# Performance work log

Hardware: AMD Instinct MI355X
Metric: run time of the kernel (lower is better)

Reference implementation:

```python
import jax, jax.numpy as jnp
import numpy as np

N_RBF = 16
N_HIDDEN = 64
CUTOFF = 5.0
N_ATOMS = 4096


def setup_inputs() -> dict:
    key = jax.random.key(0)
    ks = jax.random.split(key, 7)
    # Scale positions so the 5.0 cutoff yields a sparse-ish neighbor graph.
    positions = jax.random.normal(ks[0], (N_ATOMS, 3), dtype=jnp.float32) * 10.0
    s1 = 1.0 / np.sqrt(N_RBF)
    s2 = 1.0 / np.sqrt(N_HIDDEN)
    W1 = jax.random.normal(ks[1], (N_RBF, N_HIDDEN), dtype=jnp.float32) * s1
    b1 = jax.random.normal(ks[2], (N_HIDDEN,), dtype=jnp.float32) * 0.01
    W2 = jax.random.normal(ks[3], (N_HIDDEN, N_HIDDEN), dtype=jnp.float32) * s2
    b2 = jax.random.normal(ks[4], (N_HIDDEN,), dtype=jnp.float32) * 0.01
    W3 = jax.random.normal(ks[5], (N_HIDDEN, 1), dtype=jnp.float32) * s2
    b3 = jax.random.normal(ks[6], (1,), dtype=jnp.float32) * 0.01
    return {"positions": positions, "W1": W1, "b1": b1, "W2": W2, "b2": b2, "W3": W3, "b3": b3}


def _features(positions):
    # positions: (N, 3) -> per-node RBF-aggregated features (N, n_rbf).
    # Equivalent to torch mask.nonzero + scatter_add: features[i] = sum_j in-cutoff rbf(d_ij).
    diff = positions[:, None, :] - positions[None, :, :]          # (N, N, 3)
    dist = jnp.sqrt(jnp.sum(diff * diff, axis=-1))                # (N, N)
    mask = (dist > 1e-6) & (dist < CUTOFF)                        # (N, N)
    centers = jnp.linspace(0.5, CUTOFF, N_RBF, dtype=jnp.float32) # (n_rbf,)
    eta = 0.5 * CUTOFF / N_RBF
    gauss = jnp.exp(-((dist[..., None] - centers) ** 2) / (2.0 * eta * eta))  # (N, N, n_rbf)
    x = jnp.minimum(dist / CUTOFF, 1.0)
    smooth = 0.5 * (1.0 + jnp.cos(jnp.float32(np.pi) * x))        # (N, N)
    w = jnp.where(mask, smooth, 0.0)                              # masked smooth-cutoff weight
    return jnp.einsum('ij,ijk->ik', w, gauss)                     # (N, n_rbf)


def reference(positions, W1, b1, W2, b2, W3, b3):
    feats = _features(positions)                                  # (N, n_rbf)
    h = jax.nn.silu(feats @ W1 + b1)
    h = jax.nn.silu(h @ W2 + b2)
    energy = jnp.sum(h @ W3 + b3)                                 # scalar
    return energy
```

## Files before the change

### kernel.cpp

```cpp
#include <hip/hip_runtime.h>

#define N_ATOMS  4096
#define N_RBF    16
#define N_HIDDEN 64
#define NTHREADS 512
#define WPB      8
#define NBLOCKS  (N_ATOMS / WPB)
#define QCAP     256

__global__ void zero_out_kernel(float* __restrict__ out) {
    if (threadIdx.x == 0 && blockIdx.x == 0) out[0] = 0.0f;
}

__device__ __forceinline__ void accum_rbf(float d2, float (&f)[N_RBF]) {
    const float d  = sqrtf(d2);
    const float sm = 0.5f + 0.5f * __cosf(0.62831853071795865f * d);
    #pragma unroll
    for (int k = 0; k < N_RBF; ++k) {
        const float t = d - (0.5f + 0.3f * (float)k);
        f[k] += sm * __expf(-20.48f * t * t);
    }
}

__device__ __forceinline__ int wave_prefix(unsigned long long m) {
    return __builtin_amdgcn_mbcnt_hi((unsigned)(m >> 32),
            __builtin_amdgcn_mbcnt_lo((unsigned)m, 0u));
}

__global__ __launch_bounds__(NTHREADS, 4) void fused_sr_kernel(
    const float* __restrict__ pos,
    const float* __restrict__ W1,
    const float* __restrict__ b1,
    const float* __restrict__ W2,
    const float* __restrict__ b2,
    const float* __restrict__ W3,
    const float* __restrict__ b3,
    float* __restrict__ out)
{
    __shared__ __align__(16) float4 sp[N_ATOMS];
    __shared__ float qd[WPB][QCAP];
    __shared__ __align__(16) float h1buf[WPB][N_HIDDEN];
    __shared__ float ered[WPB];

    const int tid = threadIdx.x;

    for (int idx = tid; idx < N_ATOMS; idx += NTHREADS) {
        sp[idx] = make_float4(pos[idx * 3 + 0], pos[idx * 3 + 1], pos[idx * 3 + 2], 0.0f);
    }
    __syncthreads();

    const int lane = tid & 63;
    const int wib  = tid >> 6;
    const int i    = blockIdx.x * WPB + wib;

    const float4 pi4 = sp[i];
    const float xi = pi4.x, yi = pi4.y, zi = pi4.z;

    int cnt = 0;
    #pragma unroll 8
    for (int j0 = 0; j0 < N_ATOMS; j0 += 64) {
        const float4 pj = sp[j0 + lane];
        const float dx = xi - pj.x;
        const float dy = yi - pj.y;
        const float dz = zi - pj.z;
        const float d2 = fmaf(dx, dx, fmaf(dy, dy, dz * dz));
        const bool act = (d2 < 25.0f) && (d2 > 1e-12f);
        const unsigned long long m = __ballot(act);
        int widx = cnt + wave_prefix(m);
        widx = widx < QCAP ? widx : QCAP - 1;
        if (act) qd[wib][widx] = d2;
        cnt += (int)__popcll(m);
    }

    float f[N_RBF];
    #pragma unroll
    for (int k = 0; k < N_RBF; ++k) f[k] = 0.0f;
    for (int b = 0; b < cnt; b += 64) {
        const int q = b + lane;
        accum_rbf((q < cnt) ? qd[wib][q] : 1e8f, f);
    }

    #pragma unroll
    for (int k = 0; k < N_RBF; ++k) {
        #pragma unroll
        for (int off = 32; off > 0; off >>= 1)
            f[k] += __shfl_xor(f[k], off, 64);
    }

    float a1 = b1[lane];
    #pragma unroll
    for (int k = 0; k < N_RBF; ++k)
        a1 = fmaf(f[k], W1[k * N_HIDDEN + lane], a1);
    const float h1 = a1 / (1.0f + __expf(-a1));

    h1buf[wib][lane] = h1;
    float a2 = b2[lane];
    #pragma unroll
    for (int k = 0; k < N_HIDDEN; k += 4) {
        const float4 hv = *reinterpret_cast<const float4*>(&h1buf[wib][k]);
        a2 = fmaf(hv.x, W2[(k + 0) * N_HIDDEN + lane], a2);
        a2 = fmaf(hv.y, W2[(k + 1) * N_HIDDEN + lane], a2);
        a2 = fmaf(hv.z, W2[(k + 2) * N_HIDDEN + lane], a2);
        a2 = fmaf(hv.w, W2[(k + 3) * N_HIDDEN + lane], a2);
    }
    const float h2 = a2 / (1.0f + __expf(-a2));

    float energy = h2 * W3[lane];
    #pragma unroll
    for (int off = 32; off > 0; off >>= 1)
        energy += __shfl_xor(energy, off, 64);
    if (lane == 0) ered[wib] = energy;
    __syncthreads();
    if (tid == 0) {
        float e = 0.0f;
        #pragma unroll
        for (int w = 0; w < WPB; ++w) e += ered[w];
        atomicAdd(out, e + (float)WPB * b3[0]);
    }
}

extern "C" void kernel_launch(void* const* d_in, const int* in_sizes, int n_in,
                              void* d_out, int out_size, void* d_ws, size_t ws_size,
                              hipStream_t stream) {
    const float* pos = (const float*)d_in[0];
    const float* W1  = (const float*)d_in[1];
    const float* b1  = (const float*)d_in[2];
    const float* W2  = (const float*)d_in[3];
    const float* b2  = (const float*)d_in[4];
    const float* W3  = (const float*)d_in[5];
    const float* b3  = (const float*)d_in[6];
    float* out = (float*)d_out;

    zero_out_kernel<<<1, 64, 0, stream>>>(out);
    fused_sr_kernel<<<NBLOCKS, NTHREADS, 0, stream>>>(pos, W1, b1, W2, b2, W3, b3, out);
}
```

Before: 84.08 us.

## Split each atom's neighbor scan across two waves per atom

Each atom's neighbor scan over all positions is split between two waves, each covering half of the j range. The block grows to 1024 threads and still handles 8 atoms, so the block count is unchanged. Partial RBF sums meet in shared memory, and only the first wave of each pair runs the MLP. The intent is to halve the serial scan per wave and raise the number of resident waves for latency hiding. In exchange it adds an extra block barrier, shrinks the per-wave queue capacity and tightens the launch bounds, which may pressure registers.

```diff
diff --git a/kernel.cpp b/kernel.cpp
--- a/kernel.cpp
+++ b/kernel.cpp
@@ -3,10 +3,12 @@
 #define N_ATOMS  4096
 #define N_RBF    16
 #define N_HIDDEN 64
-#define NTHREADS 512
-#define WPB      8
-#define NBLOCKS  (N_ATOMS / WPB)
-#define QCAP     256
+#define NTHREADS 1024
+#define WPB      16
+#define APB      8
+#define NBLOCKS  (N_ATOMS / APB)
+#define QCAP     192
+#define HALF_J   (N_ATOMS / 2)
 
 __global__ void zero_out_kernel(float* __restrict__ out) {
     if (threadIdx.x == 0 && blockIdx.x == 0) out[0] = 0.0f;
@@ -27,7 +29,7 @@
             __builtin_amdgcn_mbcnt_lo((unsigned)m, 0u));
 }
 
-__global__ __launch_bounds__(NTHREADS, 4) void fused_sr_kernel(
+__global__ __launch_bounds__(NTHREADS, 8) void fused_sr_kernel(
     const float* __restrict__ pos,
     const float* __restrict__ W1,
     const float* __restrict__ b1,
@@ -38,9 +40,9 @@
     float* __restrict__ out)
 {
     __shared__ __align__(16) float4 sp[N_ATOMS];
-    __shared__ float qd[WPB][QCAP];
-    __shared__ __align__(16) float h1buf[WPB][N_HIDDEN];
-    __shared__ float ered[WPB];
+    __shared__ __align__(16) float qd[WPB][QCAP];
+    __shared__ float pairbuf[APB][2][N_RBF];
+    __shared__ float ered[APB];
 
     const int tid = threadIdx.x;
 
@@ -51,15 +53,18 @@
 
     const int lane = tid & 63;
     const int wib  = tid >> 6;
-    const int i    = blockIdx.x * WPB + wib;
+    const int pid  = wib >> 1;
+    const int half = wib & 1;
+    const int i    = blockIdx.x * APB + pid;
 
     const float4 pi4 = sp[i];
     const float xi = pi4.x, yi = pi4.y, zi = pi4.z;
 
     int cnt = 0;
-    #pragma unroll 8
-    for (int j0 = 0; j0 < N_ATOMS; j0 += 64) {
-        const float4 pj = sp[j0 + lane];
+    const int jbase = half * HALF_J;
+    #pragma unroll 4
+    for (int j0 = 0; j0 < HALF_J; j0 += 64) {
+        const float4 pj = sp[jbase + j0 + lane];
         const float dx = xi - pj.x;
         const float dy = yi - pj.y;
         const float dz = zi - pj.z;
@@ -87,35 +92,44 @@
             f[k] += __shfl_xor(f[k], off, 64);
     }
 
-    float a1 = b1[lane];
-    #pragma unroll
-    for (int k = 0; k < N_RBF; ++k)
-        a1 = fmaf(f[k], W1[k * N_HIDDEN + lane], a1);
-    const float h1 = a1 / (1.0f + __expf(-a1));
+    if (lane == 0) {
+        #pragma unroll
+        for (int k = 0; k < N_RBF; ++k) pairbuf[pid][half][k] = f[k];
+    }
+    __syncthreads();
 
-    h1buf[wib][lane] = h1;
-    float a2 = b2[lane];
-    #pragma unroll
-    for (int k = 0; k < N_HIDDEN; k += 4) {
-        const float4 hv = *reinterpret_cast<const float4*>(&h1buf[wib][k]);
-        a2 = fmaf(hv.x, W2[(k + 0) * N_HIDDEN + lane], a2);
-        a2 = fmaf(hv.y, W2[(k + 1) * N_HIDDEN + lane], a2);
-        a2 = fmaf(hv.z, W2[(k + 2) * N_HIDDEN + lane], a2);
-        a2 = fmaf(hv.w, W2[(k + 3) * N_HIDDEN + lane], a2);
+    if (half == 0) {
+        float a1 = b1[lane];
+        #pragma unroll
+        for (int k = 0; k < N_RBF; ++k)
+            a1 = fmaf(f[k] + pairbuf[pid][1][k], W1[k * N_HIDDEN + lane], a1);
+        const float h1 = a1 / (1.0f + __expf(-a1));
+
+        float* h1p = &qd[pid][0];
+        h1p[lane] = h1;
+        float a2 = b2[lane];
+        #pragma unroll
+        for (int k = 0; k < N_HIDDEN; k += 4) {
+            const float4 hv = *reinterpret_cast<const float4*>(&h1p[k]);
+            a2 = fmaf(hv.x, W2[(k + 0) * N_HIDDEN + lane], a2);
+            a2 = fmaf(hv.y, W2[(k + 1) * N_HIDDEN + lane], a2);
+            a2 = fmaf(hv.z, W2[(k + 2) * N_HIDDEN + lane], a2);
+            a2 = fmaf(hv.w, W2[(k + 3) * N_HIDDEN + lane], a2);
+        }
+        const float h2 = a2 / (1.0f + __expf(-a2));
+
+        float e = h2 * W3[lane];
+        #pragma unroll
+        for (int off = 32; off > 0; off >>= 1)
+            e += __shfl_xor(e, off, 64);
+        if (lane == 0) ered[pid] = e;
     }
-    const float h2 = a2 / (1.0f + __expf(-a2));
-
-    float energy = h2 * W3[lane];
-    #pragma unroll
-    for (int off = 32; off > 0; off >>= 1)
-        energy += __shfl_xor(energy, off, 64);
-    if (lane == 0) ered[wib] = energy;
     __syncthreads();
     if (tid == 0) {
-        float e = 0.0f;
+        float acc = 0.0f;
         #pragma unroll
-        for (int w = 0; w < WPB; ++w) e += ered[w];
-        atomicAdd(out, e + (float)WPB * b3[0]);
+        for (int w = 0; w < APB; ++w) acc += ered[w];
+        atomicAdd(out, acc + (float)APB * b3[0]);
     }
 }
 
```

New measurement: 86.29 us. 2.6% more time.
